# Kernel optimization log

Measured on AMD Instinct MI355X. Metric: run time of the kernel, lower is better.

## Reference

```python
import math
import jax, jax.numpy as jnp
import numpy as np

B, S, D = 4, 4096, 1024

def setup_inputs() -> dict:
    key = jax.random.key(0)
    ks = jax.random.split(key, 4)
    scale = 1.0 / math.sqrt(D)
    return {
        "x": jax.random.normal(ks[0], (B, S, D), dtype=jnp.float32),
        "Wq": jax.random.normal(ks[1], (D, D), dtype=jnp.float32) * scale,
        "bq": jnp.zeros((D,), dtype=jnp.float32),
        "Wk": jax.random.normal(ks[2], (D, D), dtype=jnp.float32) * scale,
        "bk": jnp.zeros((D,), dtype=jnp.float32),
        "Wv": jax.random.normal(ks[3], (D, D), dtype=jnp.float32) * scale,
        "bv": jnp.zeros((D,), dtype=jnp.float32),
    }

def reference(x, Wq, bq, Wk, bk, Wv, bv):
    # Linear layers (torch nn.Linear: x @ W.T + b)
    Q = jnp.einsum('bsd,ed->bse', x, Wq) + bq  # [B,S,D]
    K = jnp.einsum('bsd,ed->bse', x, Wk) + bk
    V = jnp.einsum('bsd,ed->bse', x, Wv) + bv
    # Full (non-flash) attention, scaled by sqrt(hidden_dim) as in source
    scores = jnp.einsum('bqd,bkd->bqk', Q, K) / jnp.sqrt(jnp.float32(Q.shape[-1]))
    attn = jax.nn.softmax(scores, axis=-1)  # [B,S,S]
    return jnp.einsum('bqk,bkd->bqd', attn, V)
```

## Files before the change

kernel.cpp:

```cpp
#include <hip/hip_runtime.h>
#include <hip/hip_bf16.h>
#include <stdint.h>


typedef __attribute__((ext_vector_type(4))) float f32x4;
typedef __attribute__((ext_vector_type(8))) short s16x8;
typedef __attribute__((ext_vector_type(4))) unsigned short u16x4;
typedef unsigned int u32;
typedef unsigned short u16;

__device__ __forceinline__ u16 f2b(float f) {
  u32 u = __float_as_uint(f);
  u = (u + 0x7FFFu + ((u >> 16) & 1u)) >> 16;
  return (u16)u;
}
__device__ __forceinline__ float b2f(u16 h) {
  return __uint_as_float(((u32)h) << 16);
}

__device__ __forceinline__ void gload_lds16(const void* g, void* l) {
  __builtin_amdgcn_global_load_lds(
      (const __attribute__((address_space(1))) void*)(const void*)g,
      (__attribute__((address_space(3))) void*)(void*)l, 16, 0, 0);
}

#define BARRIER() asm volatile("s_barrier" ::: "memory")
#define WAITLGKM0() asm volatile("s_waitcnt lgkmcnt(0)" ::: "memory")
#define WAITVM4() asm volatile("s_waitcnt vmcnt(4)" ::: "memory")
#define WAITVM0() asm volatile("s_waitcnt vmcnt(0)" ::: "memory")

__global__ __launch_bounds__(256) void k_cvt(const float* __restrict__ in,
                                             u16* __restrict__ out, int n4) {
  int i = blockIdx.x * 256 + threadIdx.x;
  if (i >= n4) return;
  f32x4 f = ((const f32x4*)in)[i];
  u16x4 h;
#pragma unroll
  for (int j = 0; j < 4; ++j) h[j] = f2b(f[j]);
  ((u16x4*)out)[i] = h;
}

template <int MODE>
__global__ __launch_bounds__(512)
void k_gemm256(const u16* __restrict__ A, const u16* __restrict__ B, int lda,
               int ldb, int K, const float* __restrict__ bias,
               void* __restrict__ Cv, int ldc, float scale, size_t az,
               size_t bz, size_t czb) {
  extern __shared__ __align__(16) u16 lds[];

  A += (size_t)blockIdx.z * az;
  B += (size_t)blockIdx.z * bz;
  char* C = (char*)Cv + (size_t)blockIdx.z * czb;

  const int gx = gridDim.x;
  const int nwg = gx * gridDim.y;
  const int bid = blockIdx.y * gx + blockIdx.x;
  const int q = nwg >> 3, r = nwg & 7;
  const int xcd = bid & 7, idx = bid >> 3;
  const int tile = (xcd < r ? xcd * (q + 1) : r * (q + 1) + (xcd - r) * q) + idx;
  const int m0 = (tile / gx) * 256;
  const int n0 = (tile % gx) * 256;

  const int tid = threadIdx.x;
  const int lane = tid & 63;
  const int wid = tid >> 6;
  const int wm = wid >> 2;
  const int wn = wid & 3;

  const int srow = lane >> 3;
  const int gcol = (((lane & 7) ^ srow) << 3);
  const int rA = lane & 15;
  const int kq = (lane >> 4) << 3;
  const int xr = (lane & 7) << 3;

#define STAGE_A(h, kt, b)                                                    \
  do {                                                                       \
    _Pragma("unroll") for (int j = 0; j < 2; ++j)                            \
        gload_lds16(A + (size_t)(m0 + (h)*128 + j * 64 + wid * 8 + srow) *   \
                            lda + (kt)*64 + gcol,                            \
                    &lds[(b)*32768 + (h)*8192 + j * 4096 + wid * 512]);      \
  } while (0)
#define STAGE_B(h, kt, b)                                                    \
  do {                                                                       \
    _Pragma("unroll") for (int j = 0; j < 2; ++j)                            \
        gload_lds16(B + (size_t)(n0 + (h)*128 + j * 64 + wid * 8 + srow) *   \
                            ldb + (kt)*64 + gcol,                            \
                    &lds[(b)*32768 + 16384 + (h)*8192 + j * 4096 +           \
                         wid * 512]);                                        \
  } while (0)
#define RD_A(dst, b, sub)                                                    \
  do {                                                                       \
    _Pragma("unroll") for (int mi = 0; mi < 4; ++mi)                         \
        _Pragma("unroll") for (int ks = 0; ks < 2; ++ks)                     \
            dst[mi][ks] = *(const s16x8*)&lds[(b)*32768 +                    \
                (wm * 128 + (sub) + mi * 16 + rA) * 64 +                     \
                ((ks * 32 + kq) ^ xr)];                                      \
  } while (0)
#define RD_B(dst, b, sub)                                                    \
  do {                                                                       \
    _Pragma("unroll") for (int ni = 0; ni < 2; ++ni)                         \
        _Pragma("unroll") for (int ks = 0; ks < 2; ++ks)                     \
            dst[ni][ks] = *(const s16x8*)&lds[(b)*32768 + 16384 +            \
                (wn * 64 + (sub) + ni * 16 + rA) * 64 +                      \
                ((ks * 32 + kq) ^ xr)];                                      \
  } while (0)
#define MM(AF, BF, MO, NO)                                                   \
  do {                                                                       \
    _Pragma("unroll") for (int mi = 0; mi < 4; ++mi)                         \
        _Pragma("unroll") for (int ni = 0; ni < 2; ++ni)                     \
            _Pragma("unroll") for (int ks = 0; ks < 2; ++ks)                 \
                acc[(MO) + mi][(NO) + ni] =                                  \
                    __builtin_amdgcn_mfma_f32_16x16x32_bf16(                 \
                        AF[mi][ks], BF[ni][ks], acc[(MO) + mi][(NO) + ni],   \
                        0, 0, 0);                                            \
  } while (0)

  f32x4 acc[8][4] = {};
  const int NT = K >> 6;

  STAGE_A(0, 0, 0);
  STAGE_A(1, 0, 0);
  STAGE_B(0, 0, 0);
  STAGE_B(1, 0, 0);
  if (NT > 1) {
    STAGE_A(0, 1, 1);
    STAGE_A(1, 1, 1);
    WAITVM4();
  } else {
    WAITVM0();
  }
  BARRIER();

  s16x8 af0[4][2], af1[4][2], bf0[2][2], bf1[2][2];
  for (int t = 0; t < NT; ++t) {
    const int b = t & 1;
    RD_A(af0, b, 0);
    RD_B(bf0, b, 0);
    if (t + 1 < NT) STAGE_B(0, t + 1, b ^ 1);
    BARRIER();
    WAITLGKM0();
    __builtin_amdgcn_s_setprio(1);
    MM(af0, bf0, 0, 0);
    __builtin_amdgcn_s_setprio(0);
    BARRIER();
    RD_A(af1, b, 64);
    if (t + 1 < NT) STAGE_B(1, t + 1, b ^ 1);
    BARRIER();
    WAITLGKM0();
    __builtin_amdgcn_s_setprio(1);
    MM(af1, bf0, 4, 0);
    __builtin_amdgcn_s_setprio(0);
    BARRIER();
    RD_B(bf1, b, 32);
    if (t + 2 < NT) STAGE_A(0, t + 2, b);
    BARRIER();
    WAITLGKM0();
    __builtin_amdgcn_s_setprio(1);
    MM(af0, bf1, 0, 2);
    __builtin_amdgcn_s_setprio(0);
    BARRIER();
    if (t + 2 < NT) STAGE_A(1, t + 2, b);
    BARRIER();
    WAITLGKM0();
    __builtin_amdgcn_s_setprio(1);
    MM(af1, bf1, 4, 2);
    __builtin_amdgcn_s_setprio(0);
    if (t + 2 < NT) {
      WAITVM4();
    } else {
      WAITVM0();
    }
    BARRIER();
  }

  const int r4 = (lane >> 4) * 4;
#pragma unroll
  for (int nj = 0; nj < 4; ++nj) {
    const int col = n0 + wn * 64 + nj * 16 + (lane & 15);
    float bcol = 0.0f;
    if (MODE == 0) bcol = bias[col];
#pragma unroll
    for (int mi = 0; mi < 8; ++mi) {
#pragma unroll
      for (int rr = 0; rr < 4; ++rr) {
        const int row = m0 + wm * 128 + mi * 16 + r4 + rr;
        float v = acc[mi][nj][rr];
        if (MODE == 0) v += bcol;
        if (MODE == 1) v += bias[row];
        if (MODE == 0 || MODE == 1) {
          ((u16*)C)[(size_t)row * ldc + col] = f2b(v);
        } else if (MODE == 2) {
          ((u16*)C)[(size_t)row * ldc + col] = f2b(v * scale);
        } else {
          ((float*)C)[(size_t)row * ldc + col] = v;
        }
      }
    }
  }
#undef STAGE_A
#undef STAGE_B
#undef RD_A
#undef RD_B
#undef MM
}

__global__ __launch_bounds__(256) void k_softmax(u16* __restrict__ S) {
  __shared__ float redm[4], reds[4];
  const int tid = threadIdx.x;
  const int lane = tid & 63;
  const int wid = tid >> 6;
  u16* sr = S + (size_t)blockIdx.x * 4096;
  s16x8 v[2];
#pragma unroll
  for (int i = 0; i < 2; ++i) v[i] = ((const s16x8*)sr)[i * 256 + tid];
  float f[16];
#pragma unroll
  for (int i = 0; i < 2; ++i)
#pragma unroll
    for (int j = 0; j < 8; ++j) f[i * 8 + j] = b2f((u16)v[i][j]);
  float m = -3.0e38f;
#pragma unroll
  for (int i = 0; i < 16; ++i) m = fmaxf(m, f[i]);
#pragma unroll
  for (int o = 32; o > 0; o >>= 1) m = fmaxf(m, __shfl_xor(m, o, 64));
  if (lane == 0) redm[wid] = m;
  __syncthreads();
  m = fmaxf(fmaxf(redm[0], redm[1]), fmaxf(redm[2], redm[3]));
  float s = 0.f;
#pragma unroll
  for (int i = 0; i < 16; ++i) {
    f[i] = __expf(f[i] - m);
    s += f[i];
  }
#pragma unroll
  for (int o = 32; o > 0; o >>= 1) s += __shfl_xor(s, o, 64);
  if (lane == 0) reds[wid] = s;
  __syncthreads();
  s = reds[0] + reds[1] + reds[2] + reds[3];
  const float inv = 1.0f / s;
#pragma unroll
  for (int i = 0; i < 2; ++i) {
    s16x8 h;
#pragma unroll
    for (int j = 0; j < 8; ++j) h[j] = (short)f2b(f[i * 8 + j] * inv);
    ((s16x8*)sr)[i * 256 + tid] = h;
  }
}

extern "C" void kernel_launch(void* const* d_in, const int* in_sizes, int n_in,
                              void* d_out, int out_size, void* d_ws,
                              size_t ws_size, hipStream_t stream) {
  const float* x = (const float*)d_in[0];
  const float* Wq = (const float*)d_in[1];
  const float* bq = (const float*)d_in[2];
  const float* Wk = (const float*)d_in[3];
  const float* bk = (const float*)d_in[4];
  const float* Wv = (const float*)d_in[5];
  const float* bv = (const float*)d_in[6];
  float* out = (float*)d_out;
  char* ws = (char*)d_ws;

  const size_t MB = 1ull << 20;
  u16* Qb = (u16*)(ws + 0 * MB);
  u16* Kb = (u16*)(ws + 32 * MB);
  u16* VtAll = (u16*)(ws + 64 * MB);
  u16* Xb = (u16*)(ws + 96 * MB);
  u16* Sc = (u16*)(ws + 96 * MB);
  u16* Wqb = (u16*)(ws + 224 * MB);
  u16* Wkb = Wqb + 1048576;
  u16* Wvb = Wqb + 2097152;

  static bool attr_set = false;
  if (!attr_set) {
    hipFuncSetAttribute((const void*)k_gemm256<0>,
                        hipFuncAttributeMaxDynamicSharedMemorySize, 131072);
    hipFuncSetAttribute((const void*)k_gemm256<1>,
                        hipFuncAttributeMaxDynamicSharedMemorySize, 131072);
    hipFuncSetAttribute((const void*)k_gemm256<2>,
                        hipFuncAttributeMaxDynamicSharedMemorySize, 131072);
    hipFuncSetAttribute((const void*)k_gemm256<3>,
                        hipFuncAttributeMaxDynamicSharedMemorySize, 131072);
    attr_set = true;
  }

  k_cvt<<<16384, 256, 0, stream>>>(x, Xb, 4194304);
  k_cvt<<<1024, 256, 0, stream>>>(Wq, Wqb, 262144);
  k_cvt<<<1024, 256, 0, stream>>>(Wk, Wkb, 262144);
  k_cvt<<<1024, 256, 0, stream>>>(Wv, Wvb, 262144);

  dim3 blk(512);
  const size_t LDSB = 131072;
  k_gemm256<0><<<dim3(4, 64, 1), blk, LDSB, stream>>>(
      Xb, Wqb, 1024, 1024, 1024, bq, Qb, 1024, 1.f, 0, 0, 0);
  k_gemm256<0><<<dim3(4, 64, 1), blk, LDSB, stream>>>(
      Xb, Wkb, 1024, 1024, 1024, bk, Kb, 1024, 1.f, 0, 0, 0);
  k_gemm256<1><<<dim3(64, 4, 1), blk, LDSB, stream>>>(
      Wvb, Xb, 1024, 1024, 1024, bv, VtAll, 16384, 1.f, 0, 0, 0);
  k_gemm256<2><<<dim3(16, 16, 4), blk, LDSB, stream>>>(
      Qb, Kb, 1024, 1024, 1024, nullptr, Sc, 4096, 0.03125f, 4194304, 4194304,
      (size_t)4096 * 4096 * 2);
  k_softmax<<<16384, 256, 0, stream>>>(Sc);
  k_gemm256<3><<<dim3(4, 16, 4), blk, LDSB, stream>>>(
      Sc, VtAll, 4096, 16384, 4096, nullptr, out, 1024, 1.f, 16777216, 4096,
      (size_t)4096 * 1024 * 4);
}
```

Measured before the change: 481.2 us.

## Prefetch LDS fragments with partial lgkmcnt waits and batch Q/K projections

Reorders the GEMM main loop so A/B fragment reads from LDS are issued earlier and only waited on partially (lgkmcnt 8/4/0) with scheduling barriers, letting MFMAs overlap outstanding LDS reads; the MFMA loop order is changed to put k-step outermost. Also merges the Q and K projection GEMMs into one launch over the z grid dimension with per-z bias selection. The cost targeted is LDS latency stalls and a separate kernel launch, at the risk of higher register pressure and fragile waitcnt accounting.

```diff
diff --git a/kernel.cpp b/kernel.cpp
--- a/kernel.cpp
+++ b/kernel.cpp
@@ -25,9 +25,12 @@
 }
 
 #define BARRIER() asm volatile("s_barrier" ::: "memory")
-#define WAITLGKM0() asm volatile("s_waitcnt lgkmcnt(0)" ::: "memory")
-#define WAITVM4() asm volatile("s_waitcnt vmcnt(4)" ::: "memory")
-#define WAITVM0() asm volatile("s_waitcnt vmcnt(0)" ::: "memory")
+#define WAITLGKM(N) \
+  do { \
+    asm volatile("s_waitcnt lgkmcnt(" #N ")" ::: "memory"); \
+    __builtin_amdgcn_sched_barrier(0); \
+  } while (0)
+#define WAITVM(N) asm volatile("s_waitcnt vmcnt(" #N ")" ::: "memory")
 
 __global__ __launch_bounds__(256) void k_cvt(const float* __restrict__ in,
                                              u16* __restrict__ out, int n4) {
@@ -44,13 +47,14 @@
 __global__ __launch_bounds__(512)
 void k_gemm256(const u16* __restrict__ A, const u16* __restrict__ B, int lda,
                int ldb, int K, const float* __restrict__ bias,
-               void* __restrict__ Cv, int ldc, float scale, size_t az,
-               size_t bz, size_t czb) {
+               const float* __restrict__ biasB, void* __restrict__ Cv, int ldc,
+               float scale, size_t az, size_t bz, size_t czb) {
   extern __shared__ __align__(16) u16 lds[];
 
   A += (size_t)blockIdx.z * az;
   B += (size_t)blockIdx.z * bz;
   char* C = (char*)Cv + (size_t)blockIdx.z * czb;
+  const float* bi = (MODE == 0 && blockIdx.z != 0) ? biasB : bias;
 
   const int gx = gridDim.x;
   const int nwg = gx * gridDim.y;
@@ -106,9 +110,9 @@
   } while (0)
 #define MM(AF, BF, MO, NO)                                                   \
   do {                                                                       \
-    _Pragma("unroll") for (int mi = 0; mi < 4; ++mi)                         \
-        _Pragma("unroll") for (int ni = 0; ni < 2; ++ni)                     \
-            _Pragma("unroll") for (int ks = 0; ks < 2; ++ks)                 \
+    _Pragma("unroll") for (int ks = 0; ks < 2; ++ks)                         \
+        _Pragma("unroll") for (int mi = 0; mi < 4; ++mi)                     \
+            _Pragma("unroll") for (int ni = 0; ni < 2; ++ni)                 \
                 acc[(MO) + mi][(NO) + ni] =                                  \
                     __builtin_amdgcn_mfma_f32_16x16x32_bf16(                 \
                         AF[mi][ks], BF[ni][ks], acc[(MO) + mi][(NO) + ni],   \
@@ -125,9 +129,9 @@
   if (NT > 1) {
     STAGE_A(0, 1, 1);
     STAGE_A(1, 1, 1);
-    WAITVM4();
+    WAITVM(4);
   } else {
-    WAITVM0();
+    WAITVM(0);
   }
   BARRIER();
 
@@ -136,39 +140,38 @@
     const int b = t & 1;
     RD_A(af0, b, 0);
     RD_B(bf0, b, 0);
+    RD_A(af1, b, 64);
     if (t + 1 < NT) STAGE_B(0, t + 1, b ^ 1);
     BARRIER();
-    WAITLGKM0();
+    WAITLGKM(8);
     __builtin_amdgcn_s_setprio(1);
     MM(af0, bf0, 0, 0);
     __builtin_amdgcn_s_setprio(0);
     BARRIER();
-    RD_A(af1, b, 64);
+    RD_B(bf1, b, 32);
     if (t + 1 < NT) STAGE_B(1, t + 1, b ^ 1);
     BARRIER();
-    WAITLGKM0();
+    WAITLGKM(4);
     __builtin_amdgcn_s_setprio(1);
     MM(af1, bf0, 4, 0);
     __builtin_amdgcn_s_setprio(0);
     BARRIER();
-    RD_B(bf1, b, 32);
     if (t + 2 < NT) STAGE_A(0, t + 2, b);
     BARRIER();
-    WAITLGKM0();
+    WAITLGKM(0);
     __builtin_amdgcn_s_setprio(1);
     MM(af0, bf1, 0, 2);
     __builtin_amdgcn_s_setprio(0);
     BARRIER();
     if (t + 2 < NT) STAGE_A(1, t + 2, b);
     BARRIER();
-    WAITLGKM0();
     __builtin_amdgcn_s_setprio(1);
     MM(af1, bf1, 4, 2);
     __builtin_amdgcn_s_setprio(0);
     if (t + 2 < NT) {
-      WAITVM4();
+      WAITVM(4);
     } else {
-      WAITVM0();
+      WAITVM(0);
     }
     BARRIER();
   }
@@ -178,7 +181,7 @@
   for (int nj = 0; nj < 4; ++nj) {
     const int col = n0 + wn * 64 + nj * 16 + (lane & 15);
     float bcol = 0.0f;
-    if (MODE == 0) bcol = bias[col];
+    if (MODE == 0) bcol = bi[col];
 #pragma unroll
     for (int mi = 0; mi < 8; ++mi) {
 #pragma unroll
@@ -186,7 +189,7 @@
         const int row = m0 + wm * 128 + mi * 16 + r4 + rr;
         float v = acc[mi][nj][rr];
         if (MODE == 0) v += bcol;
-        if (MODE == 1) v += bias[row];
+        if (MODE == 1) v += bi[row];
         if (MODE == 0 || MODE == 1) {
           ((u16*)C)[(size_t)row * ldc + col] = f2b(v);
         } else if (MODE == 2) {
@@ -270,18 +273,14 @@
   u16* Wkb = Wqb + 1048576;
   u16* Wvb = Wqb + 2097152;
 
-  static bool attr_set = false;
-  if (!attr_set) {
-    hipFuncSetAttribute((const void*)k_gemm256<0>,
-                        hipFuncAttributeMaxDynamicSharedMemorySize, 131072);
-    hipFuncSetAttribute((const void*)k_gemm256<1>,
-                        hipFuncAttributeMaxDynamicSharedMemorySize, 131072);
-    hipFuncSetAttribute((const void*)k_gemm256<2>,
-                        hipFuncAttributeMaxDynamicSharedMemorySize, 131072);
-    hipFuncSetAttribute((const void*)k_gemm256<3>,
-                        hipFuncAttributeMaxDynamicSharedMemorySize, 131072);
-    attr_set = true;
-  }
+  hipFuncSetAttribute((const void*)k_gemm256<0>,
+                      hipFuncAttributeMaxDynamicSharedMemorySize, 131072);
+  hipFuncSetAttribute((const void*)k_gemm256<1>,
+                      hipFuncAttributeMaxDynamicSharedMemorySize, 131072);
+  hipFuncSetAttribute((const void*)k_gemm256<2>,
+                      hipFuncAttributeMaxDynamicSharedMemorySize, 131072);
+  hipFuncSetAttribute((const void*)k_gemm256<3>,
+                      hipFuncAttributeMaxDynamicSharedMemorySize, 131072);
 
   k_cvt<<<16384, 256, 0, stream>>>(x, Xb, 4194304);
   k_cvt<<<1024, 256, 0, stream>>>(Wq, Wqb, 262144);
@@ -290,17 +289,16 @@
 
   dim3 blk(512);
   const size_t LDSB = 131072;
-  k_gemm256<0><<<dim3(4, 64, 1), blk, LDSB, stream>>>(
-      Xb, Wqb, 1024, 1024, 1024, bq, Qb, 1024, 1.f, 0, 0, 0);
-  k_gemm256<0><<<dim3(4, 64, 1), blk, LDSB, stream>>>(
-      Xb, Wkb, 1024, 1024, 1024, bk, Kb, 1024, 1.f, 0, 0, 0);
+  k_gemm256<0><<<dim3(4, 64, 2), blk, LDSB, stream>>>(
+      Xb, Wqb, 1024, 1024, 1024, bq, bk, Qb, 1024, 1.f, 0, 1048576,
+      (size_t)32 * MB);
   k_gemm256<1><<<dim3(64, 4, 1), blk, LDSB, stream>>>(
-      Wvb, Xb, 1024, 1024, 1024, bv, VtAll, 16384, 1.f, 0, 0, 0);
+      Wvb, Xb, 1024, 1024, 1024, bv, nullptr, VtAll, 16384, 1.f, 0, 0, 0);
   k_gemm256<2><<<dim3(16, 16, 4), blk, LDSB, stream>>>(
-      Qb, Kb, 1024, 1024, 1024, nullptr, Sc, 4096, 0.03125f, 4194304, 4194304,
-      (size_t)4096 * 4096 * 2);
+      Qb, Kb, 1024, 1024, 1024, nullptr, nullptr, Sc, 4096, 0.03125f, 4194304,
+      4194304, (size_t)4096 * 4096 * 2);
   k_softmax<<<16384, 256, 0, stream>>>(Sc);
   k_gemm256<3><<<dim3(4, 16, 4), blk, LDSB, stream>>>(
-      Sc, VtAll, 4096, 16384, 4096, nullptr, out, 1024, 1.f, 16777216, 4096,
-      (size_t)4096 * 1024 * 4);
-}
+      Sc, VtAll, 4096, 16384, 4096, nullptr, nullptr, out, 1024, 1.f, 16777216,
+      4096, (size_t)4096 * 1024 * 4);
+}
```

Measured after the change: 516.7 us. 1.07x slower.
